# Kernel optimization log

Measured on AMD Instinct MI355X. Metric: run time of the kernel, lower is better.

## Reference

```python
import jax, jax.numpy as jnp
import numpy as np

N, E, B, H, L = 100000, 200000, 2048, 256, 4
EPS_MSG = 1e-7   # GENConv message eps
LN_EPS = 1e-5    # torch LayerNorm default eps
SM_EPS = 1e-16   # PyG softmax denominator eps


def layer_norm(x, g, b):
    mu = x.mean(-1, keepdims=True)
    var = ((x - mu) ** 2).mean(-1, keepdims=True)
    return (x - mu) * jax.lax.rsqrt(var + LN_EPS) * g + b


def gen_conv(x, src, dst, eattr, t, W1, b1, lg, lb, W2, b2):
    # GENConv(aggr='softmax', learn_t, num_layers=2, norm='layer')
    msg = jax.nn.relu(x[src] + eattr) + EPS_MSG                      # [E,H]
    scaled = msg * t
    seg_max = jax.ops.segment_max(scaled, dst, num_segments=N)       # [N,H]
    seg_max = jnp.where(jnp.isfinite(seg_max), seg_max, 0.0)
    ex = jnp.exp(scaled - seg_max[dst])                              # [E,H]
    denom = jax.ops.segment_sum(ex, dst, num_segments=N)             # [N,H]
    alpha = ex / (denom[dst] + SM_EPS)
    out = jax.ops.segment_sum(msg * alpha, dst, num_segments=N)      # [N,H]
    out = out + x                                                    # root residual inside GENConv
    h = jax.nn.relu(layer_norm(out @ W1 + b1, lg, lb))               # MLP: Lin -> LN -> ReLU -> Lin
    return h @ W2 + b2


def setup_inputs() -> dict:
    key = jax.random.key(0)
    ks = iter(jax.random.split(key, 16))
    s = lambda *sh: jax.random.normal(next(ks), sh, jnp.float32) * 0.05
    return dict(
        x=jax.random.normal(next(ks), (N, 9), jnp.float32),
        edge_index=jax.random.randint(next(ks), (2, E), 0, N),
        edge_attr=jax.random.normal(next(ks), (E, 3), jnp.float32),
        batch=jnp.sort(jax.random.randint(next(ks), (N,), 0, B)),
        node_W=s(9, H), node_b=jnp.zeros((H,), jnp.float32),
        edge_W=s(3, H), edge_b=jnp.zeros((H,), jnp.float32),
        vn_emb=jnp.zeros((1, H), jnp.float32),
        ln_g=jnp.ones((L, H), jnp.float32), ln_b=jnp.zeros((L, H), jnp.float32),
        t=jnp.ones((L - 1,), jnp.float32),
        mlp_W1=s(L - 1, H, 2 * H), mlp_b1=jnp.zeros((L - 1, 2 * H), jnp.float32),
        mlp_ln_g=jnp.ones((L - 1, 2 * H), jnp.float32), mlp_ln_b=jnp.zeros((L - 1, 2 * H), jnp.float32),
        mlp_W2=s(L - 1, 2 * H, H), mlp_b2=jnp.zeros((L - 1, H), jnp.float32),
    )


def reference(x, edge_index, edge_attr, batch, node_W, node_b, edge_W, edge_b,
              vn_emb, ln_g, ln_b, t, mlp_W1, mlp_b1, mlp_ln_g, mlp_ln_b, mlp_W2, mlp_b2):
    src, dst = edge_index[0], edge_index[1]
    h = x @ node_W + node_b                                          # node encoder
    ea = edge_attr @ edge_W + edge_b                                 # edge encoder
    vn = jnp.broadcast_to(vn_emb, (B, H))
    counts = jax.ops.segment_sum(jnp.ones((N,), h.dtype), batch, num_segments=B)
    inv_counts = (1.0 / jnp.maximum(counts, 1.0))[:, None]           # [B,1]
    # layers[1:] run conv (block='res+'); layers[0] supplies only the final norm+act
    for l in range(1, L):
        hn = jax.nn.relu(layer_norm(h, ln_g[l], ln_b[l]))            # dropout=0.1 is a no-op in eval
        h = h + gen_conv(hn, src, dst, ea, t[l - 1],
                         mlp_W1[l - 1], mlp_b1[l - 1], mlp_ln_g[l - 1], mlp_ln_b[l - 1],
                         mlp_W2[l - 1], mlp_b2[l - 1])
        vn = vn + jax.ops.segment_sum(h, batch, num_segments=B) * inv_counts  # scatter_mean
        h = h + vn[batch]                                            # broadcast virtual node
    h = jax.nn.relu(layer_norm(h, ln_g[0], ln_b[0]))
    return jax.ops.segment_sum(h, batch, num_segments=B) * inv_counts  # global_mean_pool [B,H]
```

## Files before the change

### kernel.cpp

```cpp
#include <hip/hip_runtime.h>
#include <cstdint>
#include <cstddef>


typedef _Float16 half8_t __attribute__((ext_vector_type(8)));
typedef _Float16 half4_t __attribute__((ext_vector_type(4)));
typedef float    floatx4 __attribute__((ext_vector_type(4)));

#define DEVINL __device__ __forceinline__

DEVINL float wave_sum(float v) {
#pragma unroll
  for (int m = 32; m; m >>= 1) v += __shfl_xor(v, m, 64);
  return v;
}

__global__ __launch_bounds__(256) void k_node_enc(
    const float* __restrict__ x, const float* __restrict__ W,
    const float* __restrict__ bias, _Float16* __restrict__ h, int Nr) {
  __shared__ float sW[9 * 256];
  __shared__ float sb[256];
  __shared__ float sx[72];
  const int j = threadIdx.x;
#pragma unroll
  for (int k = 0; k < 9; ++k) sW[k * 256 + j] = W[k * 256 + j];
  sb[j] = bias[j];
  const int row0 = blockIdx.x * 8;
  if (j < 72) {
    int p = row0 * 9 + j;
    sx[j] = (p < Nr * 9) ? x[p] : 0.f;
  }
  __syncthreads();
  for (int r = 0; r < 8; ++r) {
    int row = row0 + r;
    if (row >= Nr) break;
    float acc = sb[j];
#pragma unroll
    for (int k = 0; k < 9; ++k) acc = fmaf(sx[r * 9 + k], sW[k * 256 + j], acc);
    h[(size_t)row * 256 + j] = (_Float16)acc;
  }
}

__global__ void k_bptr(const int* __restrict__ batch, int* __restrict__ bptr,
                       int N_, int B_) {
  int b = blockIdx.x * 256 + threadIdx.x;
  if (b > B_) return;
  int lo = 0, hi = N_;
  while (lo < hi) {
    int mid = (lo + hi) >> 1;
    if (batch[mid] < b) lo = mid + 1; else hi = mid;
  }
  bptr[b] = lo;
}

__global__ void k_deg(const int* __restrict__ ei, int* __restrict__ deg, int E_) {
  int e = blockIdx.x * 256 + threadIdx.x;
  if (e < E_) atomicAdd(&deg[ei[E_ + e]], 1);
}

__global__ __launch_bounds__(256) void k_scan1(
    const int* __restrict__ in, int* __restrict__ out1, int* __restrict__ bsum, int n) {
  __shared__ int tmp[256];
  const int t = threadIdx.x;
  const int base = blockIdx.x * 1024;
  int v[4];
  int run = 0;
#pragma unroll
  for (int i = 0; i < 4; ++i) {
    int p = base + t * 4 + i;
    int xv = (p < n) ? in[p] : 0;
    run += xv;
    v[i] = run;
  }
  tmp[t] = run;
  __syncthreads();
  for (int off = 1; off < 256; off <<= 1) {
    int u = (t >= off) ? tmp[t - off] : 0;
    __syncthreads();
    tmp[t] += u;
    __syncthreads();
  }
  int excl = tmp[t] - run;
#pragma unroll
  for (int i = 0; i < 4; ++i) {
    int p = base + t * 4 + i;
    if (p < n) out1[p] = v[i] + excl;
  }
  if (t == 255) bsum[blockIdx.x] = tmp[255];
}

__global__ void k_scan2(int* bsum, int nb, int* ptr0) {
  if (threadIdx.x == 0 && blockIdx.x == 0) {
    int run = 0;
    for (int i = 0; i < nb; ++i) { int xv = bsum[i]; bsum[i] = run; run += xv; }
    ptr0[0] = 0;
  }
}

__global__ __launch_bounds__(256) void k_scan3(int* out1, const int* __restrict__ bsum, int n) {
  int add = bsum[blockIdx.x];
  int p0 = blockIdx.x * 1024 + threadIdx.x * 4;
#pragma unroll
  for (int i = 0; i < 4; ++i) {
    int p = p0 + i;
    if (p < n) out1[p] += add;
  }
}

__global__ void k_copy(const int* __restrict__ a, int* __restrict__ b, int n) {
  int i = blockIdx.x * 256 + threadIdx.x;
  if (i < n) b[i] = a[i];
}

__global__ void k_csrfill(const int* __restrict__ ei, int* __restrict__ cursor,
                          int* __restrict__ csr_src, int* __restrict__ csr_eid, int E_) {
  int e = blockIdx.x * 256 + threadIdx.x;
  if (e < E_) {
    int d = ei[E_ + e];
    int pos = atomicAdd(&cursor[d], 1);
    csr_src[pos] = ei[e];
    csr_eid[pos] = e;
  }
}

__global__ void k_vninit(const float* __restrict__ emb, float* __restrict__ vn) {
  vn[(size_t)blockIdx.x * 256 + threadIdx.x] = emb[threadIdx.x];
}

__global__ __launch_bounds__(256) void k_wcvt_all(
    const float* __restrict__ W1, const float* __restrict__ W2,
    _Float16* __restrict__ W1T, _Float16* __restrict__ W2T) {
  int idx = blockIdx.x * 256 + threadIdx.x;
  int mat = idx >> 17;
  int rem = idx & 131071;
  if (mat < 3) {
    int k = rem >> 9, n = rem & 511;
    W1T[(size_t)mat * 131072 + (size_t)n * 256 + k] =
        (_Float16)W1[(size_t)mat * 131072 + rem];
  } else {
    int m = mat - 3;
    int k = rem >> 8, n = rem & 255;
    W2T[(size_t)m * 131072 + (size_t)n * 512 + k] =
        (_Float16)W2[(size_t)m * 131072 + rem];
  }
}

__global__ __launch_bounds__(256) void k_ln256(
    const _Float16* __restrict__ h, const float* __restrict__ g,
    const float* __restrict__ b, _Float16* __restrict__ out, int Nr) {
  int row = blockIdx.x * 4 + (threadIdx.x >> 6);
  if (row >= Nr) return;
  int lane = threadIdx.x & 63;
  half4_t xh = *(const half4_t*)(h + (size_t)row * 256 + lane * 4);
  float x0 = (float)xh[0], x1 = (float)xh[1], x2 = (float)xh[2], x3 = (float)xh[3];
  float s = wave_sum(x0 + x1 + x2 + x3);
  float mu = s * (1.f / 256.f);
  float d0 = x0 - mu, d1 = x1 - mu, d2 = x2 - mu, d3 = x3 - mu;
  float v = wave_sum(d0 * d0 + d1 * d1 + d2 * d2 + d3 * d3);
  float rstd = rsqrtf(v * (1.f / 256.f) + 1e-5f);
  float4 gv = *(const float4*)(g + lane * 4);
  float4 bv = *(const float4*)(b + lane * 4);
  half4_t o;
  o[0] = (_Float16)fmaxf(d0 * rstd * gv.x + bv.x, 0.f);
  o[1] = (_Float16)fmaxf(d1 * rstd * gv.y + bv.y, 0.f);
  o[2] = (_Float16)fmaxf(d2 * rstd * gv.z + bv.z, 0.f);
  o[3] = (_Float16)fmaxf(d3 * rstd * gv.w + bv.w, 0.f);
  *(half4_t*)(out + (size_t)row * 256 + lane * 4) = o;
}

__global__ __launch_bounds__(256) void k_aggregate(
    const _Float16* __restrict__ hn, const float* __restrict__ eattr,
    const float* __restrict__ edgeW, const float* __restrict__ edgeB,
    const int* __restrict__ indptr, const int* __restrict__ csr_src,
    const int* __restrict__ csr_eid, const float* __restrict__ tptr,
    _Float16* __restrict__ agg, int Nr) {
  int node = blockIdx.x * 4 + (threadIdx.x >> 6);
  if (node >= Nr) return;
  int lane = threadIdx.x & 63;
  int j0 = lane * 4;
  float4 w0 = *(const float4*)(edgeW + j0);
  float4 w1 = *(const float4*)(edgeW + 256 + j0);
  float4 w2 = *(const float4*)(edgeW + 512 + j0);
  float4 wb = *(const float4*)(edgeB + j0);
  float W0[4] = {w0.x, w0.y, w0.z, w0.w};
  float W1r[4] = {w1.x, w1.y, w1.z, w1.w};
  float W2r[4] = {w2.x, w2.y, w2.z, w2.w};
  float WB[4] = {wb.x, wb.y, wb.z, wb.w};
  float tval = tptr[0];
  int e0 = indptr[node], e1 = indptr[node + 1];
  float D[4] = {0.f, 0.f, 0.f, 0.f};
  float Nu[4] = {0.f, 0.f, 0.f, 0.f};
  for (int s = e0; s < e1; ++s) {
    int srcn = csr_src[s];
    int eid = csr_eid[s];
    float ex0 = eattr[(size_t)eid * 3 + 0];
    float ex1 = eattr[(size_t)eid * 3 + 1];
    float ex2 = eattr[(size_t)eid * 3 + 2];
    half4_t hv = *(const half4_t*)(hn + (size_t)srcn * 256 + j0);
#pragma unroll
    for (int i = 0; i < 4; ++i) {
      float eaj = fmaf(ex0, W0[i], fmaf(ex1, W1r[i], fmaf(ex2, W2r[i], WB[i])));
      float msg = fmaxf((float)hv[i] + eaj, 0.f) + 1e-7f;
      float pr = __expf(msg * tval);
      D[i] += pr;
      Nu[i] = fmaf(pr, msg, Nu[i]);
    }
  }
  half4_t hs = *(const half4_t*)(hn + (size_t)node * 256 + j0);
  half4_t res;
#pragma unroll
  for (int i = 0; i < 4; ++i)
    res[i] = (_Float16)(Nu[i] / (D[i] + 1e-16f) + (float)hs[i]);
  *(half4_t*)(agg + (size_t)node * 256 + j0) = res;
}

template <int VN>
__global__ __launch_bounds__(512, 2) void k_fused(
    const _Float16* __restrict__ A, const _Float16* __restrict__ B1T,
    const float* __restrict__ b1, const float* __restrict__ lg,
    const float* __restrict__ lb, const _Float16* __restrict__ B2T,
    const float* __restrict__ b2, const float* __restrict__ vn,
    const int* __restrict__ batch, _Float16* __restrict__ outf, int M) {
  __shared__ _Float16 ldsT1[64 * 512];
  __shared__ _Float16 ldsS[2048 * 8];
  __shared__ _Float16 ldsB1[1024 * 8];
  __shared__ float sb1[512];
  __shared__ float sg[512];
  __shared__ float sbt[512];
  __shared__ float sb2[256];
  __shared__ float sstat[64 * 4];

  const int tid = threadIdx.x;
  const int lane = tid & 63;
  const int wv = tid >> 6;
  const int q = lane >> 4;
  const int l16 = lane & 15;
  const int m0 = blockIdx.x * 64;
  const int wm = (wv >> 1) * 16;
  const int cg = wv & 1;

  sb1[tid] = b1[tid];
  sg[tid] = lg[tid];
  sbt[tid] = lb[tid];
  if (tid < 256) sb2[tid] = b2[tid];

  {
    half8_t tmp[4];
    int ss[4];
#pragma unroll
    for (int g = 0; g < 4; ++g) {
      int s = g * 512 + tid;
      int r = s >> 5;
      int c = (s & 31) ^ (r & 7);
      int rowA = m0 + r;
      rowA = rowA < M ? rowA : (M - 1);
      tmp[g] = *(const half8_t*)(A + (size_t)rowA * 256 + c * 8);
      ss[g] = s;
    }
#pragma unroll
    for (int g = 0; g < 4; ++g)
      *(half8_t*)(ldsS + (size_t)ss[g] * 8) = tmp[g];
  }

  size_t offB[2];
  int ldsOffB[2];
#pragma unroll
  for (int i = 0; i < 2; ++i) {
    int p = i * 512 + tid;
    int r = p >> 3;
    int s = p & 7;
    int gg = s ^ (r & 7);
    offB[i] = (size_t)r * 256 + gg * 8;
    ldsOffB[i] = p * 8;
  }
  half8_t rb[2];
  auto loadB1 = [&](int j) {
    int n = j >> 2, t = j & 3;
    size_t base = (size_t)n * 128 * 256 + (size_t)t * 64;
#pragma unroll
    for (int i = 0; i < 2; ++i)
      rb[i] = *(const half8_t*)(B1T + base + offB[i]);
  };
  auto writeB1 = [&]() {
#pragma unroll
    for (int i = 0; i < 2; ++i)
      *(half8_t*)(ldsB1 + ldsOffB[i]) = rb[i];
  };

  floatx4 acc[4] = {};
  float sA[4] = {0.f, 0.f, 0.f, 0.f}, s2A[4] = {0.f, 0.f, 0.f, 0.f};
  const int wn1 = cg * 64;

  loadB1(0);
  writeB1();
  for (int j = 0; j < 16; ++j) {
    __syncthreads();
    if (j + 1 < 16) loadB1(j + 1);
    const int t = j & 3;
#pragma unroll
    for (int kk = 0; kk < 2; ++kk) {
      const int c8 = kk * 4 + q;
      const int ck = t * 8 + c8;
      int r = wm + l16;
      half8_t af = *(const half8_t*)(ldsS + (size_t)(r * 32 + (ck ^ (r & 7))) * 8);
      half8_t bf[4];
#pragma unroll
      for (int ct = 0; ct < 4; ++ct) {
        int n = wn1 + ct * 16 + l16;
        bf[ct] = *(const half8_t*)(ldsB1 + (size_t)(n * 8 + (c8 ^ (n & 7))) * 8);
      }
#pragma unroll
      for (int ct = 0; ct < 4; ++ct)
        acc[ct] = __builtin_amdgcn_mfma_f32_16x16x32_f16(af, bf[ct], acc[ct], 0, 0, 0);
    }
    __syncthreads();
    if (j + 1 < 16) writeB1();
    if ((j & 3) == 3) {
      int n = j >> 2;
#pragma unroll
      for (int rr = 0; rr < 4; ++rr) {
        int rloc = wm + q * 4 + rr;
#pragma unroll
        for (int ct = 0; ct < 4; ++ct) {
          int col = n * 128 + wn1 + ct * 16 + l16;
          float v = acc[ct][rr] + sb1[col];
          sA[rr] += v;
          s2A[rr] += v * v;
          int cch = col >> 3;
          int slot = (cch & 56) | ((cch & 7) ^ (rloc & 7));
          ldsT1[(size_t)rloc * 512 + slot * 8 + (col & 7)] = (_Float16)v;
        }
      }
#pragma unroll
      for (int ct = 0; ct < 4; ++ct) acc[ct] = floatx4{0.f, 0.f, 0.f, 0.f};
    }
  }

#pragma unroll
  for (int rr = 0; rr < 4; ++rr) {
    float s = sA[rr], s2 = s2A[rr];
#pragma unroll
    for (int m = 1; m < 16; m <<= 1) {
      s += __shfl_xor(s, m, 64);
      s2 += __shfl_xor(s2, m, 64);
    }
    if (l16 == 0) {
      int rloc = wm + q * 4 + rr;
      sstat[rloc * 4 + cg * 2 + 0] = s;
      sstat[rloc * 4 + cg * 2 + 1] = s2;
    }
  }

  size_t offB2[4];
  int ldsOffB2[4];
#pragma unroll
  for (int i = 0; i < 4; ++i) {
    int p = i * 512 + tid;
    int r = p >> 3;
    int s = p & 7;
    int gg = s ^ (r & 7);
    offB2[i] = (size_t)r * 512 + gg * 8;
    ldsOffB2[i] = p * 8;
  }
  half8_t rb2[4];
  auto loadB2 = [&](int kt) {
#pragma unroll
    for (int i = 0; i < 4; ++i)
      rb2[i] = *(const half8_t*)(B2T + offB2[i] + kt * 64);
  };
  auto writeB2 = [&]() {
#pragma unroll
    for (int i = 0; i < 4; ++i)
      *(half8_t*)(ldsS + ldsOffB2[i]) = rb2[i];
  };

  loadB2(0);
  __syncthreads();
  writeB2();

  {
    int r = tid >> 3;
    int t7 = tid & 7;
    float fs = sstat[r * 4 + 0] + sstat[r * 4 + 2];
    float fs2 = sstat[r * 4 + 1] + sstat[r * 4 + 3];
    float mu = fs * (1.f / 512.f);
    float var = fs2 * (1.f / 512.f) - mu * mu;
    float rs = rsqrtf(var + 1e-5f);
#pragma unroll
    for (int g = 0; g < 8; ++g) {
      int slot = g * 8 + t7;
      int cch = (slot & 56) | ((slot & 7) ^ (r & 7));
      half8_t v = *(half8_t*)(ldsT1 + (size_t)r * 512 + slot * 8);
      half8_t o;
      int c0 = cch * 8;
#pragma unroll
      for (int jj = 0; jj < 8; ++jj) {
        float e = ((float)v[jj] - mu) * rs;
        o[jj] = (_Float16)fmaxf(fmaf(e, sg[c0 + jj], sbt[c0 + jj]), 0.f);
      }
      *(half8_t*)(ldsT1 + (size_t)r * 512 + slot * 8) = o;
    }
  }

  floatx4 acc2[8] = {};
  const int wn2 = cg * 128;
  for (int kt = 0; kt < 8; ++kt) {
    __syncthreads();
    if (kt + 1 < 8) loadB2(kt + 1);
#pragma unroll
    for (int kk = 0; kk < 2; ++kk) {
      const int c8 = kk * 4 + q;
      int r = wm + l16;
      half8_t af = *(const half8_t*)(ldsT1 + (size_t)(r * 64 + kt * 8 + (c8 ^ (r & 7))) * 8);
      half8_t bf[8];
#pragma unroll
      for (int ct = 0; ct < 8; ++ct) {
        int n = wn2 + ct * 16 + l16;
        bf[ct] = *(const half8_t*)(ldsS + (size_t)(n * 8 + (c8 ^ (n & 7))) * 8);
      }
#pragma unroll
      for (int ct = 0; ct < 8; ++ct)
        acc2[ct] = __builtin_amdgcn_mfma_f32_16x16x32_f16(af, bf[ct], acc2[ct], 0, 0, 0);
    }
    __syncthreads();
    if (kt + 1 < 8) writeB2();
  }

  constexpr int EPS2 = 136;
  _Float16* epi = ldsT1 + (size_t)wv * (16 * EPS2);
#pragma unroll
  for (int rr = 0; rr < 4; ++rr) {
    int rloc = q * 4 + rr;
    int row = m0 + wm + rloc;
    int rowc = row < M ? row : (M - 1);
    int bb = 0;
    if constexpr (VN) bb = batch[rowc];
#pragma unroll
    for (int ct = 0; ct < 8; ++ct) {
      int cloc = ct * 16 + l16;
      int col = wn2 + cloc;
      float v = acc2[ct][rr] + sb2[col];
      if constexpr (VN) v += vn[(size_t)bb * 256 + col];
      epi[rloc * EPS2 + cloc] = (_Float16)v;
    }
  }
#pragma unroll
  for (int it = 0; it < 4; ++it) {
    int rloc = it * 4 + (lane >> 4);
    int row = m0 + wm + rloc;
    if (row < M) {
      int c0 = (lane & 15) * 8;
      size_t gidx = (size_t)row * 256 + wn2 + c0;
      half8_t hv = *(const half8_t*)(outf + gidx);
      half8_t ev = *(const half8_t*)(epi + rloc * EPS2 + c0);
      half8_t o;
#pragma unroll
      for (int jj = 0; jj < 8; ++jj) o[jj] = (_Float16)((float)hv[jj] + (float)ev[jj]);
      *(half8_t*)(outf + gidx) = o;
    }
  }
}

__global__ __launch_bounds__(256) void k_vnln(
    const _Float16* __restrict__ h, float* __restrict__ vn,
    const int* __restrict__ bptr, const float* __restrict__ g,
    const float* __restrict__ b, _Float16* __restrict__ hn) {
  __shared__ float red[3][256];
  __shared__ float svn[256];
  int bb = blockIdx.x;
  int w = threadIdx.x >> 6;
  int lane = threadIdx.x & 63;
  int n0 = bptr[bb], n1 = bptr[bb + 1];
  float a0 = 0.f, a1 = 0.f, a2 = 0.f, a3 = 0.f;
  for (int row = n0 + w; row < n1; row += 4) {
    half4_t xh = *(const half4_t*)(h + (size_t)row * 256 + lane * 4);
    a0 += (float)xh[0]; a1 += (float)xh[1];
    a2 += (float)xh[2]; a3 += (float)xh[3];
  }
  if (w > 0) {
    red[w - 1][lane * 4 + 0] = a0;
    red[w - 1][lane * 4 + 1] = a1;
    red[w - 1][lane * 4 + 2] = a2;
    red[w - 1][lane * 4 + 3] = a3;
  }
  __syncthreads();
  if (w == 0) {
    int c = n1 - n0;
    float ic = 1.f / (float)(c > 1 ? c : 1);
#pragma unroll
    for (int k = 0; k < 3; ++k) {
      a0 += red[k][lane * 4 + 0];
      a1 += red[k][lane * 4 + 1];
      a2 += red[k][lane * 4 + 2];
      a3 += red[k][lane * 4 + 3];
    }
    float4 vo = *(const float4*)(vn + (size_t)bb * 256 + lane * 4);
    vo.x += a0 * ic; vo.y += a1 * ic; vo.z += a2 * ic; vo.w += a3 * ic;
    *(float4*)(vn + (size_t)bb * 256 + lane * 4) = vo;
    svn[lane * 4 + 0] = vo.x;
    svn[lane * 4 + 1] = vo.y;
    svn[lane * 4 + 2] = vo.z;
    svn[lane * 4 + 3] = vo.w;
  }
  __syncthreads();
  float4 vv = *(const float4*)(svn + lane * 4);
  float4 gv = *(const float4*)(g + lane * 4);
  float4 bv = *(const float4*)(b + lane * 4);
  for (int row = n0 + w; row < n1; row += 4) {
    half4_t xh = *(const half4_t*)(h + (size_t)row * 256 + lane * 4);
    float x0 = (float)xh[0] + vv.x, x1 = (float)xh[1] + vv.y;
    float x2 = (float)xh[2] + vv.z, x3 = (float)xh[3] + vv.w;
    float s = wave_sum(x0 + x1 + x2 + x3);
    float mu = s * (1.f / 256.f);
    float d0 = x0 - mu, d1 = x1 - mu, d2 = x2 - mu, d3 = x3 - mu;
    float v = wave_sum(d0 * d0 + d1 * d1 + d2 * d2 + d3 * d3);
    float rstd = rsqrtf(v * (1.f / 256.f) + 1e-5f);
    half4_t o;
    o[0] = (_Float16)fmaxf(d0 * rstd * gv.x + bv.x, 0.f);
    o[1] = (_Float16)fmaxf(d1 * rstd * gv.y + bv.y, 0.f);
    o[2] = (_Float16)fmaxf(d2 * rstd * gv.z + bv.z, 0.f);
    o[3] = (_Float16)fmaxf(d3 * rstd * gv.w + bv.w, 0.f);
    *(half4_t*)(hn + (size_t)row * 256 + lane * 4) = o;
  }
}

__global__ __launch_bounds__(256) void k_vnlnpool(
    const _Float16* __restrict__ h, const float* __restrict__ vn,
    const int* __restrict__ bptr, const float* __restrict__ g,
    const float* __restrict__ b, float* __restrict__ out) {
  __shared__ float red[3][256];
  __shared__ float svn[256];
  int bb = blockIdx.x;
  int w = threadIdx.x >> 6;
  int lane = threadIdx.x & 63;
  int n0 = bptr[bb], n1 = bptr[bb + 1];
  int c = n1 - n0;
  float ic = 1.f / (float)(c > 1 ? c : 1);
  float a0 = 0.f, a1 = 0.f, a2 = 0.f, a3 = 0.f;
  for (int row = n0 + w; row < n1; row += 4) {
    half4_t xh = *(const half4_t*)(h + (size_t)row * 256 + lane * 4);
    a0 += (float)xh[0]; a1 += (float)xh[1];
    a2 += (float)xh[2]; a3 += (float)xh[3];
  }
  if (w > 0) {
    red[w - 1][lane * 4 + 0] = a0;
    red[w - 1][lane * 4 + 1] = a1;
    red[w - 1][lane * 4 + 2] = a2;
    red[w - 1][lane * 4 + 3] = a3;
  }
  __syncthreads();
  if (w == 0) {
#pragma unroll
    for (int k = 0; k < 3; ++k) {
      a0 += red[k][lane * 4 + 0];
      a1 += red[k][lane * 4 + 1];
      a2 += red[k][lane * 4 + 2];
      a3 += red[k][lane * 4 + 3];
    }
    float4 vo = *(const float4*)(vn + (size_t)bb * 256 + lane * 4);
    svn[lane * 4 + 0] = vo.x + a0 * ic;
    svn[lane * 4 + 1] = vo.y + a1 * ic;
    svn[lane * 4 + 2] = vo.z + a2 * ic;
    svn[lane * 4 + 3] = vo.w + a3 * ic;
  }
  __syncthreads();
  float4 vv = *(const float4*)(svn + lane * 4);
  float4 gv = *(const float4*)(g + lane * 4);
  float4 bv = *(const float4*)(b + lane * 4);
  a0 = a1 = a2 = a3 = 0.f;
  for (int row = n0 + w; row < n1; row += 4) {
    half4_t xh = *(const half4_t*)(h + (size_t)row * 256 + lane * 4);
    float x0 = (float)xh[0] + vv.x, x1 = (float)xh[1] + vv.y;
    float x2 = (float)xh[2] + vv.z, x3 = (float)xh[3] + vv.w;
    float s = wave_sum(x0 + x1 + x2 + x3);
    float mu = s * (1.f / 256.f);
    float d0 = x0 - mu, d1 = x1 - mu, d2 = x2 - mu, d3 = x3 - mu;
    float v = wave_sum(d0 * d0 + d1 * d1 + d2 * d2 + d3 * d3);
    float rstd = rsqrtf(v * (1.f / 256.f) + 1e-5f);
    a0 += fmaxf(d0 * rstd * gv.x + bv.x, 0.f);
    a1 += fmaxf(d1 * rstd * gv.y + bv.y, 0.f);
    a2 += fmaxf(d2 * rstd * gv.z + bv.z, 0.f);
    a3 += fmaxf(d3 * rstd * gv.w + bv.w, 0.f);
  }
  __syncthreads();
  if (w > 0) {
    red[w - 1][lane * 4 + 0] = a0;
    red[w - 1][lane * 4 + 1] = a1;
    red[w - 1][lane * 4 + 2] = a2;
    red[w - 1][lane * 4 + 3] = a3;
  }
  __syncthreads();
  if (w == 0) {
#pragma unroll
    for (int k = 0; k < 3; ++k) {
      a0 += red[k][lane * 4 + 0];
      a1 += red[k][lane * 4 + 1];
      a2 += red[k][lane * 4 + 2];
      a3 += red[k][lane * 4 + 3];
    }
    float4 o = {a0 * ic, a1 * ic, a2 * ic, a3 * ic};
    *(float4*)(out + (size_t)bb * 256 + lane * 4) = o;
  }
}

extern "C" void kernel_launch(void* const* d_in, const int* in_sizes, int n_in,
                              void* d_out, int out_size, void* d_ws, size_t ws_size,
                              hipStream_t stream) {
  const float* x      = (const float*)d_in[0];
  const int*   ei     = (const int*)d_in[1];
  const float* eattr  = (const float*)d_in[2];
  const int*   batch  = (const int*)d_in[3];
  const float* nodeW  = (const float*)d_in[4];
  const float* nodeB  = (const float*)d_in[5];
  const float* edgeW  = (const float*)d_in[6];
  const float* edgeB  = (const float*)d_in[7];
  const float* vnemb  = (const float*)d_in[8];
  const float* lng    = (const float*)d_in[9];
  const float* lnb    = (const float*)d_in[10];
  const float* tparam = (const float*)d_in[11];
  const float* W1     = (const float*)d_in[12];
  const float* b1     = (const float*)d_in[13];
  const float* mlng   = (const float*)d_in[14];
  const float* mlnb   = (const float*)d_in[15];
  const float* W2     = (const float*)d_in[16];
  const float* b2     = (const float*)d_in[17];
  float* out = (float*)d_out;

  const int N = in_sizes[3];
  const int E = in_sizes[1] / 2;
  const int B = out_size / 256;

  char* p = (char*)d_ws;
  auto take = [&](size_t bytes) -> char* {
    char* r = p;
    p += (bytes + 255) & ~(size_t)255;
    return r;
  };
  _Float16*  h   = (_Float16*)take((size_t)N * 256 * 2);
  _Float16*  hn  = (_Float16*)take((size_t)N * 256 * 2);
  _Float16*  agg = (_Float16*)take((size_t)N * 256 * 2);
  _Float16*  W1T = (_Float16*)take((size_t)3 * 512 * 256 * 2);
  _Float16*  W2T = (_Float16*)take((size_t)3 * 256 * 512 * 2);
  float*     vn  = (float*)take((size_t)B * 256 * 4);
  int*       bptr   = (int*)take((size_t)(B + 1) * 4);
  int*       deg    = (int*)take((size_t)N * 4);
  int*       indptr = (int*)take((size_t)(N + 1) * 4);
  int*       cursor = (int*)take((size_t)N * 4);
  int*       csr_src = (int*)take((size_t)E * 4);
  int*       csr_eid = (int*)take((size_t)E * 4);
  int*       bsum    = (int*)take(512 * 4);
  (void)ws_size; (void)n_in;

  hipMemsetAsync(deg, 0, (size_t)N * 4, stream);

  k_node_enc<<<(N + 7) / 8, 256, 0, stream>>>(x, nodeW, nodeB, h, N);
  k_bptr<<<(B + 256) / 256, 256, 0, stream>>>(batch, bptr, N, B);

  const int nbN = (N + 1023) / 1024;
  k_deg<<<(E + 255) / 256, 256, 0, stream>>>(ei, deg, E);
  k_scan1<<<nbN, 256, 0, stream>>>(deg, indptr + 1, bsum, N);
  k_scan2<<<1, 64, 0, stream>>>(bsum, nbN, indptr);
  k_scan3<<<nbN, 256, 0, stream>>>(indptr + 1, bsum, N);
  k_copy<<<(N + 255) / 256, 256, 0, stream>>>(indptr, cursor, N);
  k_csrfill<<<(E + 255) / 256, 256, 0, stream>>>(ei, cursor, csr_src, csr_eid, E);

  k_wcvt_all<<<3072, 256, 0, stream>>>(W1, W2, W1T, W2T);
  k_vninit<<<B, 256, 0, stream>>>(vnemb, vn);

  const int lnGrid = (N + 3) / 4;
  const int mTiles = (N + 63) / 64;

  k_ln256<<<lnGrid, 256, 0, stream>>>(h, lng + 256, lnb + 256, hn, N);
  for (int l = 1; l <= 3; ++l) {
    k_aggregate<<<lnGrid, 256, 0, stream>>>(hn, eattr, edgeW, edgeB, indptr, csr_src, csr_eid,
                                            tparam + (l - 1), agg, N);
    if (l == 1)
      k_fused<0><<<mTiles, 512, 0, stream>>>(
          agg, W1T + (size_t)(l - 1) * 512 * 256, b1 + (size_t)(l - 1) * 512,
          mlng + (size_t)(l - 1) * 512, mlnb + (size_t)(l - 1) * 512,
          W2T + (size_t)(l - 1) * 256 * 512, b2 + (size_t)(l - 1) * 256,
          nullptr, nullptr, h, N);
    else
      k_fused<1><<<mTiles, 512, 0, stream>>>(
          agg, W1T + (size_t)(l - 1) * 512 * 256, b1 + (size_t)(l - 1) * 512,
          mlng + (size_t)(l - 1) * 512, mlnb + (size_t)(l - 1) * 512,
          W2T + (size_t)(l - 1) * 256 * 512, b2 + (size_t)(l - 1) * 256,
          vn, batch, h, N);
    if (l < 3)
      k_vnln<<<B, 256, 0, stream>>>(h, vn, bptr,
                                    lng + (size_t)(l + 1) * 256, lnb + (size_t)(l + 1) * 256, hn);
    else
      k_vnlnpool<<<B, 256, 0, stream>>>(h, vn, bptr, lng, lnb, out);
  }
}
```

Measured before the change: 848.4 us.

## Shrink fused MLP tile to 32 rows with 256 threads, unroll aggregate edge loop by two

The fused Lin-LN-ReLU-Lin kernel now processes 32-row tiles with 256 threads instead of 64 rows with 512. Both GEMM phases share one LDS B buffer and the second GEMM is split into two 128-column passes with a reused 4-tile accumulator. LDS per block drops and register pressure falls, so more blocks can be resident and the grid has twice as many tiles; the cost is that each weight tile is loaded from L2 by twice as many blocks. LayerNorm statistics are now reduced once per row into a scale/shift pair. The edge aggregation loop is unrolled by two so the gathers for two edges can be in flight together.

```diff
diff --git a/kernel.cpp b/kernel.cpp
--- a/kernel.cpp
+++ b/kernel.cpp
@@ -190,20 +190,46 @@
   int e0 = indptr[node], e1 = indptr[node + 1];
   float D[4] = {0.f, 0.f, 0.f, 0.f};
   float Nu[4] = {0.f, 0.f, 0.f, 0.f};
-  for (int s = e0; s < e1; ++s) {
-    int srcn = csr_src[s];
-    int eid = csr_eid[s];
-    float ex0 = eattr[(size_t)eid * 3 + 0];
-    float ex1 = eattr[(size_t)eid * 3 + 1];
-    float ex2 = eattr[(size_t)eid * 3 + 2];
-    half4_t hv = *(const half4_t*)(hn + (size_t)srcn * 256 + j0);
+  int s = e0;
+  for (; s + 2 <= e1; s += 2) {
+    int sa = csr_src[s], sb = csr_src[s + 1];
+    int ea = csr_eid[s], eb = csr_eid[s + 1];
+    float ax0 = eattr[(size_t)ea * 3 + 0];
+    float ax1 = eattr[(size_t)ea * 3 + 1];
+    float ax2 = eattr[(size_t)ea * 3 + 2];
+    float bx0 = eattr[(size_t)eb * 3 + 0];
+    float bx1 = eattr[(size_t)eb * 3 + 1];
+    float bx2 = eattr[(size_t)eb * 3 + 2];
+    half4_t ha = *(const half4_t*)(hn + (size_t)sa * 256 + j0);
+    half4_t hb = *(const half4_t*)(hn + (size_t)sb * 256 + j0);
 #pragma unroll
     for (int i = 0; i < 4; ++i) {
-      float eaj = fmaf(ex0, W0[i], fmaf(ex1, W1r[i], fmaf(ex2, W2r[i], WB[i])));
-      float msg = fmaxf((float)hv[i] + eaj, 0.f) + 1e-7f;
-      float pr = __expf(msg * tval);
-      D[i] += pr;
-      Nu[i] = fmaf(pr, msg, Nu[i]);
+      float ea_j = fmaf(ax0, W0[i], fmaf(ax1, W1r[i], fmaf(ax2, W2r[i], WB[i])));
+      float ma = fmaxf((float)ha[i] + ea_j, 0.f) + 1e-7f;
+      float pa = __expf(ma * tval);
+      D[i] += pa;
+      Nu[i] = fmaf(pa, ma, Nu[i]);
+      float eb_j = fmaf(bx0, W0[i], fmaf(bx1, W1r[i], fmaf(bx2, W2r[i], WB[i])));
+      float mb = fmaxf((float)hb[i] + eb_j, 0.f) + 1e-7f;
+      float pb = __expf(mb * tval);
+      D[i] += pb;
+      Nu[i] = fmaf(pb, mb, Nu[i]);
+    }
+  }
+  if (s < e1) {
+    int sa = csr_src[s];
+    int ea = csr_eid[s];
+    float ax0 = eattr[(size_t)ea * 3 + 0];
+    float ax1 = eattr[(size_t)ea * 3 + 1];
+    float ax2 = eattr[(size_t)ea * 3 + 2];
+    half4_t ha = *(const half4_t*)(hn + (size_t)sa * 256 + j0);
+#pragma unroll
+    for (int i = 0; i < 4; ++i) {
+      float ea_j = fmaf(ax0, W0[i], fmaf(ax1, W1r[i], fmaf(ax2, W2r[i], WB[i])));
+      float ma = fmaxf((float)ha[i] + ea_j, 0.f) + 1e-7f;
+      float pa = __expf(ma * tval);
+      D[i] += pa;
+      Nu[i] = fmaf(pa, ma, Nu[i]);
     }
   }
   half4_t hs = *(const half4_t*)(hn + (size_t)node * 256 + j0);
@@ -215,41 +241,42 @@
 }
 
 template <int VN>
-__global__ __launch_bounds__(512, 2) void k_fused(
+__global__ __launch_bounds__(256, 2) void k_fmlp(
     const _Float16* __restrict__ A, const _Float16* __restrict__ B1T,
     const float* __restrict__ b1, const float* __restrict__ lg,
     const float* __restrict__ lb, const _Float16* __restrict__ B2T,
     const float* __restrict__ b2, const float* __restrict__ vn,
     const int* __restrict__ batch, _Float16* __restrict__ outf, int M) {
-  __shared__ _Float16 ldsT1[64 * 512];
-  __shared__ _Float16 ldsS[2048 * 8];
-  __shared__ _Float16 ldsB1[1024 * 8];
+  __shared__ _Float16 ldsT1[32 * 512];
+  __shared__ _Float16 ldsA[32 * 256];
+  __shared__ _Float16 ldsB[1024 * 8];
   __shared__ float sb1[512];
   __shared__ float sg[512];
   __shared__ float sbt[512];
   __shared__ float sb2[256];
-  __shared__ float sstat[64 * 4];
+  __shared__ float sred[32 * 4];
+  __shared__ float2 sac[32];
 
   const int tid = threadIdx.x;
   const int lane = tid & 63;
   const int wv = tid >> 6;
+  const int wband = wv >> 1;
+  const int whalf = wv & 1;
   const int q = lane >> 4;
   const int l16 = lane & 15;
-  const int m0 = blockIdx.x * 64;
-  const int wm = (wv >> 1) * 16;
-  const int cg = wv & 1;
-
-  sb1[tid] = b1[tid];
-  sg[tid] = lg[tid];
-  sbt[tid] = lb[tid];
-  if (tid < 256) sb2[tid] = b2[tid];
+  const int m0 = blockIdx.x * 32;
+
+  sb1[tid] = b1[tid]; sb1[tid + 256] = b1[tid + 256];
+  sg[tid]  = lg[tid]; sg[tid + 256]  = lg[tid + 256];
+  sbt[tid] = lb[tid]; sbt[tid + 256] = lb[tid + 256];
+  sb2[tid] = b2[tid];
 
   {
     half8_t tmp[4];
     int ss[4];
 #pragma unroll
     for (int g = 0; g < 4; ++g) {
-      int s = g * 512 + tid;
+      int s = g * 256 + tid;
       int r = s >> 5;
       int c = (s & 31) ^ (r & 7);
       int rowA = m0 + r;
@@ -259,40 +286,47 @@
     }
 #pragma unroll
     for (int g = 0; g < 4; ++g)
-      *(half8_t*)(ldsS + (size_t)ss[g] * 8) = tmp[g];
-  }
-
-  size_t offB[2];
-  int ldsOffB[2];
-#pragma unroll
-  for (int i = 0; i < 2; ++i) {
-    int p = i * 512 + tid;
+      *(half8_t*)(ldsA + (size_t)ss[g] * 8) = tmp[g];
+  }
+
+  size_t offB1[4], offB2[4];
+  int ldsOffB[4];
+#pragma unroll
+  for (int i = 0; i < 4; ++i) {
+    int p = (i * 4 + wv) * 64 + lane;
     int r = p >> 3;
     int s = p & 7;
     int gg = s ^ (r & 7);
-    offB[i] = (size_t)r * 256 + gg * 8;
+    offB1[i] = (size_t)r * 256 + gg * 8;
+    offB2[i] = (size_t)r * 512 + gg * 8;
     ldsOffB[i] = p * 8;
   }
-  half8_t rb[2];
+  half8_t rb[4];
   auto loadB1 = [&](int j) {
-    int n = j >> 2, t = j & 3;
-    size_t base = (size_t)n * 128 * 256 + (size_t)t * 64;
-#pragma unroll
-    for (int i = 0; i < 2; ++i)
-      rb[i] = *(const half8_t*)(B1T + base + offB[i]);
+    int nt = j >> 2, kt = j & 3;
+    size_t base = (size_t)nt * 128 * 256 + (size_t)kt * 64;
+#pragma unroll
+    for (int i = 0; i < 4; ++i)
+      rb[i] = *(const half8_t*)(B1T + base + offB1[i]);
   };
-  auto writeB1 = [&]() {
-#pragma unroll
-    for (int i = 0; i < 2; ++i)
-      *(half8_t*)(ldsB1 + ldsOffB[i]) = rb[i];
+  auto loadB2 = [&](int j) {
+    int n2 = j >> 3, kt = j & 7;
+    size_t base = (size_t)n2 * 128 * 512 + (size_t)kt * 64;
+#pragma unroll
+    for (int i = 0; i < 4; ++i)
+      rb[i] = *(const half8_t*)(B2T + base + offB2[i]);
+  };
+  auto writeB = [&]() {
+#pragma unroll
+    for (int i = 0; i < 4; ++i)
+      *(half8_t*)(ldsB + ldsOffB[i]) = rb[i];
   };
 
   floatx4 acc[4] = {};
   float sA[4] = {0.f, 0.f, 0.f, 0.f}, s2A[4] = {0.f, 0.f, 0.f, 0.f};
-  const int wn1 = cg * 64;
 
   loadB1(0);
-  writeB1();
+  writeB();
   for (int j = 0; j < 16; ++j) {
     __syncthreads();
     if (j + 1 < 16) loadB1(j + 1);
@@ -300,36 +334,39 @@
 #pragma unroll
     for (int kk = 0; kk < 2; ++kk) {
       const int c8 = kk * 4 + q;
-      const int ck = t * 8 + c8;
-      int r = wm + l16;
-      half8_t af = *(const half8_t*)(ldsS + (size_t)(r * 32 + (ck ^ (r & 7))) * 8);
+      const int cg = t * 8 + c8;
+      int r = wband * 16 + l16;
+      half8_t af = *(const half8_t*)(ldsA + (size_t)(r * 32 + (cg ^ (r & 7))) * 8);
       half8_t bf[4];
 #pragma unroll
       for (int ct = 0; ct < 4; ++ct) {
-        int n = wn1 + ct * 16 + l16;
-        bf[ct] = *(const half8_t*)(ldsB1 + (size_t)(n * 8 + (c8 ^ (n & 7))) * 8);
+        int n = whalf * 64 + ct * 16 + l16;
+        bf[ct] = *(const half8_t*)(ldsB + (size_t)(n * 8 + (c8 ^ (n & 7))) * 8);
       }
 #pragma unroll
       for (int ct = 0; ct < 4; ++ct)
         acc[ct] = __builtin_amdgcn_mfma_f32_16x16x32_f16(af, bf[ct], acc[ct], 0, 0, 0);
     }
     __syncthreads();
-    if (j + 1 < 16) writeB1();
+    if (j + 1 < 16) writeB();
     if ((j & 3) == 3) {
-      int n = j >> 2;
+      int nt = j >> 2;
 #pragma unroll
       for (int rr = 0; rr < 4; ++rr) {
-        int rloc = wm + q * 4 + rr;
+        int rloc = wband * 16 + q * 4 + rr;
+        float s = 0.f, s2 = 0.f;
 #pragma unroll
         for (int ct = 0; ct < 4; ++ct) {
-          int col = n * 128 + wn1 + ct * 16 + l16;
+          int col = nt * 128 + whalf * 64 + ct * 16 + l16;
           float v = acc[ct][rr] + sb1[col];
-          sA[rr] += v;
-          s2A[rr] += v * v;
+          s += v;
+          s2 += v * v;
           int cch = col >> 3;
           int slot = (cch & 56) | ((cch & 7) ^ (rloc & 7));
           ldsT1[(size_t)rloc * 512 + slot * 8 + (col & 7)] = (_Float16)v;
         }
+        sA[rr] += s;
+        s2A[rr] += s2;
       }
 #pragma unroll
       for (int ct = 0; ct < 4; ++ct) acc[ct] = floatx4{0.f, 0.f, 0.f, 0.f};
@@ -345,47 +382,27 @@
       s2 += __shfl_xor(s2, m, 64);
     }
     if (l16 == 0) {
-      int rloc = wm + q * 4 + rr;
-      sstat[rloc * 4 + cg * 2 + 0] = s;
-      sstat[rloc * 4 + cg * 2 + 1] = s2;
-    }
-  }
-
-  size_t offB2[4];
-  int ldsOffB2[4];
-#pragma unroll
-  for (int i = 0; i < 4; ++i) {
-    int p = i * 512 + tid;
-    int r = p >> 3;
-    int s = p & 7;
-    int gg = s ^ (r & 7);
-    offB2[i] = (size_t)r * 512 + gg * 8;
-    ldsOffB2[i] = p * 8;
-  }
-  half8_t rb2[4];
-  auto loadB2 = [&](int kt) {
-#pragma unroll
-    for (int i = 0; i < 4; ++i)
-      rb2[i] = *(const half8_t*)(B2T + offB2[i] + kt * 64);
-  };
-  auto writeB2 = [&]() {
-#pragma unroll
-    for (int i = 0; i < 4; ++i)
-      *(half8_t*)(ldsS + ldsOffB2[i]) = rb2[i];
-  };
-
+      int rloc = wband * 16 + q * 4 + rr;
+      sred[rloc * 4 + whalf * 2 + 0] = s;
+      sred[rloc * 4 + whalf * 2 + 1] = s2;
+    }
+  }
   loadB2(0);
   __syncthreads();
-  writeB2();
+  if (tid < 32) {
+    float fs = sred[tid * 4 + 0] + sred[tid * 4 + 2];
+    float fs2 = sred[tid * 4 + 1] + sred[tid * 4 + 3];
+    float mu = fs * (1.f / 512.f);
+    float var = fs2 * (1.f / 512.f) - mu * mu;
+    float rs = rsqrtf(var + 1e-5f);
+    sac[tid] = make_float2(rs, -mu * rs);
+  }
+  __syncthreads();
 
   {
     int r = tid >> 3;
     int t7 = tid & 7;
-    float fs = sstat[r * 4 + 0] + sstat[r * 4 + 2];
-    float fs2 = sstat[r * 4 + 1] + sstat[r * 4 + 3];
-    float mu = fs * (1.f / 512.f);
-    float var = fs2 * (1.f / 512.f) - mu * mu;
-    float rs = rsqrtf(var + 1e-5f);
+    float2 ac = sac[r];
 #pragma unroll
     for (int g = 0; g < 8; ++g) {
       int slot = g * 8 + t7;
@@ -395,69 +412,74 @@
       int c0 = cch * 8;
 #pragma unroll
       for (int jj = 0; jj < 8; ++jj) {
-        float e = ((float)v[jj] - mu) * rs;
+        float e = fmaf((float)v[jj], ac.x, ac.y);
         o[jj] = (_Float16)fmaxf(fmaf(e, sg[c0 + jj], sbt[c0 + jj]), 0.f);
       }
       *(half8_t*)(ldsT1 + (size_t)r * 512 + slot * 8) = o;
     }
   }
-
-  floatx4 acc2[8] = {};
-  const int wn2 = cg * 128;
-  for (int kt = 0; kt < 8; ++kt) {
-    __syncthreads();
-    if (kt + 1 < 8) loadB2(kt + 1);
-#pragma unroll
-    for (int kk = 0; kk < 2; ++kk) {
-      const int c8 = kk * 4 + q;
-      int r = wm + l16;
-      half8_t af = *(const half8_t*)(ldsT1 + (size_t)(r * 64 + kt * 8 + (c8 ^ (r & 7))) * 8);
-      half8_t bf[8];
-#pragma unroll
-      for (int ct = 0; ct < 8; ++ct) {
-        int n = wn2 + ct * 16 + l16;
-        bf[ct] = *(const half8_t*)(ldsS + (size_t)(n * 8 + (c8 ^ (n & 7))) * 8);
+  writeB();
+
+  for (int n2 = 0; n2 < 2; ++n2) {
+#pragma unroll 1
+    for (int kt = 0; kt < 8; ++kt) {
+      __syncthreads();
+      int j2 = n2 * 8 + kt;
+      if (j2 + 1 < 16) loadB2(j2 + 1);
+#pragma unroll
+      for (int kk = 0; kk < 2; ++kk) {
+        const int c8 = kk * 4 + q;
+        const int ck = kt * 8 + c8;
+        int r = wband * 16 + l16;
+        int slot = (ck & 56) | ((ck & 7) ^ (r & 7));
+        half8_t af = *(const half8_t*)(ldsT1 + (size_t)(r * 64 + slot) * 8);
+        half8_t bf[4];
+#pragma unroll
+        for (int ct = 0; ct < 4; ++ct) {
+          int n = whalf * 64 + ct * 16 + l16;
+          bf[ct] = *(const half8_t*)(ldsB + (size_t)(n * 8 + (c8 ^ (n & 7))) * 8);
+        }
+#pragma unroll
+        for (int ct = 0; ct < 4; ++ct)
+          acc[ct] = __builtin_amdgcn_mfma_f32_16x16x32_f16(af, bf[ct], acc[ct], 0, 0, 0);
       }
-#pragma unroll
-      for (int ct = 0; ct < 8; ++ct)
-        acc2[ct] = __builtin_amdgcn_mfma_f32_16x16x32_f16(af, bf[ct], acc2[ct], 0, 0, 0);
-    }
-    __syncthreads();
-    if (kt + 1 < 8) writeB2();
-  }
-
-  constexpr int EPS2 = 136;
-  _Float16* epi = ldsT1 + (size_t)wv * (16 * EPS2);
-#pragma unroll
-  for (int rr = 0; rr < 4; ++rr) {
-    int rloc = q * 4 + rr;
-    int row = m0 + wm + rloc;
-    int rowc = row < M ? row : (M - 1);
-    int bb = 0;
-    if constexpr (VN) bb = batch[rowc];
-#pragma unroll
-    for (int ct = 0; ct < 8; ++ct) {
-      int cloc = ct * 16 + l16;
-      int col = wn2 + cloc;
-      float v = acc2[ct][rr] + sb2[col];
-      if constexpr (VN) v += vn[(size_t)bb * 256 + col];
-      epi[rloc * EPS2 + cloc] = (_Float16)v;
-    }
-  }
-#pragma unroll
-  for (int it = 0; it < 4; ++it) {
-    int rloc = it * 4 + (lane >> 4);
-    int row = m0 + wm + rloc;
-    if (row < M) {
-      int c0 = (lane & 15) * 8;
-      size_t gidx = (size_t)row * 256 + wn2 + c0;
-      half8_t hv = *(const half8_t*)(outf + gidx);
-      half8_t ev = *(const half8_t*)(epi + rloc * EPS2 + c0);
-      half8_t o;
-#pragma unroll
-      for (int jj = 0; jj < 8; ++jj) o[jj] = (_Float16)((float)hv[jj] + (float)ev[jj]);
-      *(half8_t*)(outf + gidx) = o;
-    }
+      __syncthreads();
+      if (j2 + 1 < 16) writeB();
+    }
+    _Float16* epi = ldsA + (size_t)wv * (16 * 68);
+#pragma unroll
+    for (int rr = 0; rr < 4; ++rr) {
+      int lr = q * 4 + rr;
+      int row = m0 + wband * 16 + lr;
+      int rowc = row < M ? row : (M - 1);
+      int bb = 0;
+      if constexpr (VN) bb = batch[rowc];
+#pragma unroll
+      for (int ct = 0; ct < 4; ++ct) {
+        int cloc = ct * 16 + l16;
+        int col = n2 * 128 + whalf * 64 + cloc;
+        float v = acc[ct][rr] + sb2[col];
+        if constexpr (VN) v += vn[(size_t)bb * 256 + col];
+        epi[lr * 68 + cloc] = (_Float16)v;
+      }
+    }
+#pragma unroll
+    for (int it = 0; it < 2; ++it) {
+      int lr = it * 8 + (lane >> 3);
+      int row = m0 + wband * 16 + lr;
+      if (row < M) {
+        int c0 = (lane & 7) * 8;
+        size_t gidx = (size_t)row * 256 + n2 * 128 + whalf * 64 + c0;
+        half8_t hv = *(const half8_t*)(outf + gidx);
+        half8_t ev = *(const half8_t*)(epi + lr * 68 + c0);
+        half8_t o;
+#pragma unroll
+        for (int jj = 0; jj < 8; ++jj) o[jj] = (_Float16)((float)hv[jj] + (float)ev[jj]);
+        *(half8_t*)(outf + gidx) = o;
+      }
+    }
+#pragma unroll
+    for (int ct = 0; ct < 4; ++ct) acc[ct] = floatx4{0.f, 0.f, 0.f, 0.f};
   }
 }
 
@@ -668,20 +690,20 @@
   k_vninit<<<B, 256, 0, stream>>>(vnemb, vn);
 
   const int lnGrid = (N + 3) / 4;
-  const int mTiles = (N + 63) / 64;
+  const int mTiles = (N + 31) / 32;
 
   k_ln256<<<lnGrid, 256, 0, stream>>>(h, lng + 256, lnb + 256, hn, N);
   for (int l = 1; l <= 3; ++l) {
     k_aggregate<<<lnGrid, 256, 0, stream>>>(hn, eattr, edgeW, edgeB, indptr, csr_src, csr_eid,
                                             tparam + (l - 1), agg, N);
     if (l == 1)
-      k_fused<0><<<mTiles, 512, 0, stream>>>(
+      k_fmlp<0><<<mTiles, 256, 0, stream>>>(
           agg, W1T + (size_t)(l - 1) * 512 * 256, b1 + (size_t)(l - 1) * 512,
           mlng + (size_t)(l - 1) * 512, mlnb + (size_t)(l - 1) * 512,
           W2T + (size_t)(l - 1) * 256 * 512, b2 + (size_t)(l - 1) * 256,
           nullptr, nullptr, h, N);
     else
-      k_fused<1><<<mTiles, 512, 0, stream>>>(
+      k_fmlp<1><<<mTiles, 256, 0, stream>>>(
           agg, W1T + (size_t)(l - 1) * 512 * 256, b1 + (size_t)(l - 1) * 512,
           mlng + (size_t)(l - 1) * 512, mlnb + (size_t)(l - 1) * 512,
           W2T + (size_t)(l - 1) * 256 * 512, b2 + (size_t)(l - 1) * 256,
```

New measurement: 834.7 us. No clear change (-1.6%).
